# Kernel tuning notes

Measured on AMD Instinct MI355X. Metric: run time of the kernel, lower is better.

Reference implementation:

```python
import jax, jax.numpy as jnp
import numpy as np

N, D1, D2, BW, B = 8, 1024, 1024, 3, 1024
D = D1 * D2
RES_DENOS = [3.0, 5.0, 17.0, 257.0, 65537.0]  # [2^2-1, 2^2+1, 2^4+1, 2^8+1, 2^16+1]
SPLIT_TEMP = 0.01


def ste_floor(x):
    # forward: floor, backward: identity (matches custom round autograd.Function)
    return x + jax.lax.stop_gradient(jnp.floor(x) - x)


def quantize_weights(U, thres_mean):
    beta, alpha = jnp.max(U), jnp.min(U)
    s = (beta - alpha) / RES_DENOS[0]
    vals_sum = s * ste_floor(U / s)  # level 0
    col = jnp.arange(D)[None, :]
    for idx in range(1, BW):
        s = s / RES_DENOS[idx]
        res_err = U - vals_sum                                   # [N, D]
        order = jnp.argsort(res_err, axis=0)                     # [N, D] int
        sorted_err = jnp.take_along_axis(res_err, order, axis=0) # [N, D]
        delta = sorted_err[1:] - sorted_err[:-1]                 # [N-1, D]
        delta = delta / jnp.max(delta)
        # differentiable split points, one per gap between sorted rows
        sp = jax.nn.sigmoid((jnp.mean(delta, axis=1) - jax.nn.sigmoid(thres_mean)[0]) / SPLIT_TEMP)  # [N-1]
        b = jnp.round(sp)                                        # hard 0/1 boundary (zero grad, like torch branch)
        gid = jnp.concatenate([jnp.zeros((1,), sp.dtype), jnp.cumsum(b)]).astype(jnp.int32)  # [N] group id per row
        counts = jax.ops.segment_sum(jnp.ones((N,), U.dtype), gid, num_segments=N)           # [N]
        sums = jax.ops.segment_sum(sorted_err, gid, num_segments=N)                          # [N, D]
        means = sums / jnp.maximum(counts, 1.0)[:, None]
        # grad_ factor: sp at boundary rows, (1-sp) at interior rows, 1 for the last row
        factors = jnp.where(b == 1.0, sp, 1.0 - sp)              # [N-1], in (0,1)
        logf = jnp.concatenate([jnp.log(factors), jnp.zeros((1,), sp.dtype)])  # [N]
        grad_g = jnp.exp(jax.ops.segment_sum(logf, gid, num_segments=N))       # [N] per-group product
        t = grad_g[gid][:, None] * means[gid]                    # [N, D] group value broadcast to member rows
        # scatter back through the sort permutation (== one-hot transfer matmul)
        grouped = jnp.zeros_like(U).at[order, col].set(t)
        vals_sum = vals_sum + s * ste_floor(grouped / s)
    return vals_sum


def setup_inputs() -> dict:
    key = jax.random.key(0)
    kx, ku = jax.random.split(key)
    x = jax.random.normal(kx, (B, N, D1), dtype=jnp.float32)
    # kaiming_normal_ on (N, D): std = sqrt(2 / fan_in) with fan_in = D
    U = jax.random.normal(ku, (N, D), dtype=jnp.float32) * np.sqrt(2.0 / D).astype(np.float32)
    thres_mean = jnp.array([-0.405], dtype=jnp.float32)
    return {"x": x, "U": U, "thres_mean": thres_mean}


def reference(x, U, thres_mean):
    w = quantize_weights(U, thres_mean).reshape(N, D1, D2)
    return jnp.einsum('bnd,ndl->bnl', x, w)
```

## Files before the change

### kernel.cpp

```cpp
#include <hip/hip_runtime.h>
#include <hip/hip_bf16.h>
#include <stdint.h>

#define DD (1 << 20)
#define NPART 4096

typedef float v4f __attribute__((ext_vector_type(4)));
typedef __bf16 bf16x8 __attribute__((ext_vector_type(8)));

struct Scalars {
  float s;
  int   uniform;
  float coef[8];
  float cnti[8];
  int   isend[8];
};

struct Partial {
  double g[7];
  double mx;
};

static __device__ __forceinline__ unsigned short f2bf(float v) {
  unsigned u = __float_as_uint(v);
  u += 0x7fffu + ((u >> 16) & 1u);
  return (unsigned short)(u >> 16);
}

__global__ void k_minmax_partial(const float4* __restrict__ U4, float2* __restrict__ part) {
  int tid = threadIdx.x, bid = blockIdx.x;
  float mn = 3.4e38f, mx = -3.4e38f;
#pragma unroll
  for (int j = 0; j < 8; ++j) {
    float4 v = U4[(size_t)(bid * 8 + j) * 256 + tid];
    mn = fminf(mn, fminf(fminf(v.x, v.y), fminf(v.z, v.w)));
    mx = fmaxf(mx, fmaxf(fmaxf(v.x, v.y), fmaxf(v.z, v.w)));
  }
#pragma unroll
  for (int off = 32; off; off >>= 1) {
    mn = fminf(mn, __shfl_down(mn, off, 64));
    mx = fmaxf(mx, __shfl_down(mx, off, 64));
  }
  __shared__ float2 w4[4];
  if ((tid & 63) == 0) w4[tid >> 6] = make_float2(mn, mx);
  __syncthreads();
  if (tid == 0) {
    for (int i = 1; i < 4; ++i) { mn = fminf(mn, w4[i].x); mx = fmaxf(mx, w4[i].y); }
    part[bid] = make_float2(mn, mx);
  }
}

__global__ void k_minmax_final(const float2* __restrict__ part, Scalars* sc) {
  int tid = threadIdx.x;
  float mn = 3.4e38f, mx = -3.4e38f;
#pragma unroll
  for (int j = 0; j < 4; ++j) {
    float2 p = part[j * 256 + tid];
    mn = fminf(mn, p.x); mx = fmaxf(mx, p.y);
  }
#pragma unroll
  for (int off = 32; off; off >>= 1) {
    mn = fminf(mn, __shfl_down(mn, off, 64));
    mx = fmaxf(mx, __shfl_down(mx, off, 64));
  }
  __shared__ float2 w4[4];
  if ((tid & 63) == 0) w4[tid >> 6] = make_float2(mn, mx);
  __syncthreads();
  if (tid == 0) {
    for (int i = 1; i < 4; ++i) { mn = fminf(mn, w4[i].x); mx = fmaxf(mx, w4[i].y); }
    sc->s = (mx - mn) / 3.0f;
  }
}

#define CE2(a, b)                                                        \
  { float ra = r[a], rb = r[b]; int oa = ord[a], ob = ord[b];            \
    bool sw = (ra > rb) || (ra == rb && oa > ob);                        \
    r[a] = sw ? rb : ra; r[b] = sw ? ra : rb;                            \
    ord[a] = sw ? ob : oa; ord[b] = sw ? oa : ob; }

#define SORTNET8                                                          \
  CE2(0,1) CE2(2,3) CE2(4,5) CE2(6,7)                                     \
  CE2(0,2) CE2(1,3) CE2(4,6) CE2(5,7)                                     \
  CE2(1,2) CE2(5,6)                                                       \
  CE2(0,4) CE2(1,5) CE2(2,6) CE2(3,7)                                     \
  CE2(2,4) CE2(3,5)                                                       \
  CE2(1,2) CE2(3,4) CE2(5,6)

#define CEV(a, b) { float ra = q[a], rb = q[b]; q[a] = fminf(ra, rb); q[b] = fmaxf(ra, rb); }
#define SORTNET8V                                                         \
  CEV(0,1) CEV(2,3) CEV(4,5) CEV(6,7)                                     \
  CEV(0,2) CEV(1,3) CEV(4,6) CEV(5,7)                                     \
  CEV(1,2) CEV(5,6)                                                       \
  CEV(0,4) CEV(1,5) CEV(2,6) CEV(3,7)                                     \
  CEV(2,4) CEV(3,5)                                                       \
  CEV(1,2) CEV(3,4) CEV(5,6)

static __device__ __forceinline__ void stats_block_reduce(float dl[7], float mx,
                                                          Partial* __restrict__ po) {
#pragma unroll
  for (int off = 32; off; off >>= 1) {
#pragma unroll
    for (int g = 0; g < 7; ++g) dl[g] += __shfl_down(dl[g], off, 64);
    mx = fmaxf(mx, __shfl_down(mx, off, 64));
  }
  __shared__ double wsum[4][7];
  __shared__ float wmax[4];
  int lane = threadIdx.x & 63, wv = threadIdx.x >> 6;
  if (lane == 0) {
#pragma unroll
    for (int g = 0; g < 7; ++g) wsum[wv][g] = (double)dl[g];
    wmax[wv] = mx;
  }
  __syncthreads();
  if (threadIdx.x == 0) {
#pragma unroll
    for (int g = 0; g < 7; ++g)
      po->g[g] = wsum[0][g] + wsum[1][g] + wsum[2][g] + wsum[3][g];
    po->mx = (double)fmaxf(fmaxf(wmax[0], wmax[1]), fmaxf(wmax[2], wmax[3]));
  }
}

__global__ void k_level0_stats(const float* __restrict__ U, float* __restrict__ vals,
                               Partial* __restrict__ part, const Scalars* __restrict__ sc) {
  int d = blockIdx.x * 256 + threadIdx.x;
  float s = sc->s;
  float q[8];
#pragma unroll
  for (int n = 0; n < 8; ++n) {
    size_t ix = ((size_t)n << 20) + d;
    float u = U[ix];
    float v = s * floorf(u / s);
    vals[ix] = v;
    q[n] = u - v;
  }
  SORTNET8V
  float dl[7]; float mx = 0.f;
#pragma unroll
  for (int g = 0; g < 7; ++g) { dl[g] = q[g + 1] - q[g]; mx = fmaxf(mx, dl[g]); }
  stats_block_reduce(dl, mx, &part[blockIdx.x]);
}

__global__ void k_scalars2(const Partial* __restrict__ part, Scalars* sc,
                           const float* __restrict__ thres, float deno) {
  int t = threadIdx.x;
  double g[7] = {0, 0, 0, 0, 0, 0, 0};
  double mx = 0.0;
#pragma unroll
  for (int j = 0; j < NPART / 256; ++j) {
    const Partial& p = part[j * 256 + t];
#pragma unroll
    for (int i = 0; i < 7; ++i) g[i] += p.g[i];
    mx = fmax(mx, p.mx);
  }
#pragma unroll
  for (int off = 32; off; off >>= 1) {
#pragma unroll
    for (int i = 0; i < 7; ++i) g[i] += __shfl_down(g[i], off, 64);
    mx = fmax(mx, __shfl_down(mx, off, 64));
  }
  __shared__ double sg[4][8];
  int lane = t & 63, wv = t >> 6;
  if (lane == 0) {
#pragma unroll
    for (int i = 0; i < 7; ++i) sg[wv][i] = g[i];
    sg[wv][7] = mx;
  }
  __syncthreads();
  if (t != 0) return;
#pragma unroll
  for (int i = 0; i < 7; ++i) g[i] = sg[0][i] + sg[1][i] + sg[2][i] + sg[3][i];
  mx = fmax(fmax(sg[0][7], sg[1][7]), fmax(sg[2][7], sg[3][7]));

  float s = sc->s / deno;
  sc->s = s;
  float md = (float)mx;
  float sigT = 1.f / (1.f + expf(-thres[0]));
  float sp[7], bb[7];
  for (int gg = 0; gg < 7; ++gg) {
    float mean = (float)(g[gg] / ((double)DD * (double)md));
    float z = (mean - sigT) / 0.01f;
    sp[gg] = 1.f / (1.f + expf(-z));
    bb[gg] = rintf(sp[gg]);
  }
  int gid[8]; gid[0] = 0;
  for (int i = 1; i < 8; ++i) gid[i] = gid[i - 1] + (int)bb[i - 1];
  float counts[8] = {0, 0, 0, 0, 0, 0, 0, 0};
  for (int i = 0; i < 8; ++i) counts[gid[i]] += 1.f;
  float lsum[8] = {0, 0, 0, 0, 0, 0, 0, 0};
  for (int i = 0; i < 7; ++i) {
    float f = (bb[i] == 1.f) ? sp[i] : (1.f - sp[i]);
    lsum[gid[i]] += logf(f);
  }
  float gradg[8];
  for (int gg = 0; gg < 8; ++gg) gradg[gg] = expf(lsum[gg]);
  for (int i = 0; i < 8; ++i) {
    sc->coef[i] = gradg[gid[i]];
    sc->cnti[i] = fmaxf(counts[gid[i]], 1.f);
    sc->isend[i] = (i == 7) || (gid[i + 1] != gid[i]);
  }
  sc->uniform = (gid[7] == 0) ? 1 : 0;
}

static __device__ __forceinline__ void update_core(const float u[8], const float vo[8],
                                                   const float coef[8], const float cnti[8],
                                                   const int isend[8], float s,
                                                   float vnew[8]) {
  float r[8]; int ord[8];
#pragma unroll
  for (int n = 0; n < 8; ++n) { r[n] = u[n] - vo[n]; ord[n] = n; }
  SORTNET8
  float endsum[8]; float a = 0.f;
#pragma unroll
  for (int i = 0; i < 8; ++i) { a += r[i]; endsum[i] = a; if (isend[i]) a = 0.f; }
  float t[8]; float gsv = 0.f;
#pragma unroll
  for (int i = 7; i >= 0; --i) {
    if (isend[i]) gsv = endsum[i];
    t[i] = coef[i] * (gsv / cnti[i]);
  }
#pragma unroll
  for (int n = 0; n < 8; ++n) {
    float tv = 0.f;
#pragma unroll
    for (int i = 0; i < 8; ++i) tv = (ord[i] == n) ? t[i] : tv;
    vnew[n] = vo[n] + s * floorf(tv / s);
  }
}

static __device__ __forceinline__ float uniform_delta(const float u[8], const float vo[8],
                                                      float coef0, float cnt0, float s) {
  float q[8];
#pragma unroll
  for (int n = 0; n < 8; ++n) q[n] = u[n] - vo[n];
  SORTNET8V
  float a = 0.f;
#pragma unroll
  for (int i = 0; i < 8; ++i) a += q[i];
  float t = coef0 * (a / cnt0);
  return s * floorf(t / s);
}

__global__ void k_update_stats(const float* __restrict__ U, float* __restrict__ vals,
                               Partial* __restrict__ part, const Scalars* __restrict__ sc) {
  int d = blockIdx.x * 256 + threadIdx.x;
  float s = sc->s;
  float u[8], vo[8], vnew[8];
#pragma unroll
  for (int n = 0; n < 8; ++n) {
    size_t ix = ((size_t)n << 20) + d;
    u[n] = U[ix];
    vo[n] = vals[ix];
  }
  if (sc->uniform) {
    float c = uniform_delta(u, vo, sc->coef[0], sc->cnti[0], s);
#pragma unroll
    for (int n = 0; n < 8; ++n) vnew[n] = vo[n] + c;
  } else {
    float coef[8], cnti[8]; int isend[8];
#pragma unroll
    for (int i = 0; i < 8; ++i) { coef[i] = sc->coef[i]; cnti[i] = sc->cnti[i]; isend[i] = sc->isend[i]; }
    update_core(u, vo, coef, cnti, isend, s, vnew);
  }
  float q[8];
#pragma unroll
  for (int n = 0; n < 8; ++n) {
    size_t ix = ((size_t)n << 20) + d;
    vals[ix] = vnew[n];
    q[n] = u[n] - vnew[n];
  }
  SORTNET8V
  float dl[7]; float mx = 0.f;
#pragma unroll
  for (int g = 0; g < 7; ++g) { dl[g] = q[g + 1] - q[g]; mx = fmaxf(mx, dl[g]); }
  stats_block_reduce(dl, mx, &part[blockIdx.x]);
}

__global__ void k_final_pack(const float* __restrict__ x, const float* __restrict__ U,
                             const float* __restrict__ vals, const Scalars* __restrict__ sc,
                             unsigned short* __restrict__ xT, unsigned short* __restrict__ wT) {
  __shared__ unsigned short stile[8][32][34];
  int t = threadIdx.x;
  if (blockIdx.x < 1024) {
    int k0 = (blockIdx.x >> 5) * 32;
    int l0 = (blockIdx.x & 31) * 32;
    float s = sc->s;
    int uni = sc->uniform;
    float coef0 = sc->coef[0], cnt0 = sc->cnti[0];
    int kk = t >> 3;
    int lq = t & 7;
    int d0 = (k0 + kk) * 1024 + l0 + lq * 4;
    float4 u4[8], vo4[8];
#pragma unroll
    for (int n = 0; n < 8; ++n) {
      u4[n]  = *(const float4*)(U    + ((size_t)n << 20) + d0);
      vo4[n] = *(const float4*)(vals + ((size_t)n << 20) + d0);
    }
    if (uni) {
#pragma unroll
      for (int j = 0; j < 4; ++j) {
        float u[8], vo[8];
#pragma unroll
        for (int n = 0; n < 8; ++n) { u[n] = ((const float*)&u4[n])[j]; vo[n] = ((const float*)&vo4[n])[j]; }
        float c = uniform_delta(u, vo, coef0, cnt0, s);
#pragma unroll
        for (int n = 0; n < 8; ++n) stile[n][kk][lq * 4 + j] = f2bf(vo[n] + c);
      }
    } else {
      float coef[8], cnti[8]; int isend[8];
#pragma unroll
      for (int i = 0; i < 8; ++i) { coef[i] = sc->coef[i]; cnti[i] = sc->cnti[i]; isend[i] = sc->isend[i]; }
#pragma unroll
      for (int j = 0; j < 4; ++j) {
        float u[8], vo[8], vnew[8];
#pragma unroll
        for (int n = 0; n < 8; ++n) { u[n] = ((const float*)&u4[n])[j]; vo[n] = ((const float*)&vo4[n])[j]; }
        update_core(u, vo, coef, cnti, isend, s, vnew);
#pragma unroll
        for (int n = 0; n < 8; ++n) stile[n][kk][lq * 4 + j] = f2bf(vnew[n]);
      }
    }
    __syncthreads();
    int ll = t >> 3, kq = t & 7;
#pragma unroll
    for (int n = 0; n < 8; ++n) {
      ushort4 o;
      o.x = stile[n][kq * 4 + 0][ll];
      o.y = stile[n][kq * 4 + 1][ll];
      o.z = stile[n][kq * 4 + 2][ll];
      o.w = stile[n][kq * 4 + 3][ll];
      *(ushort4*)(wT + ((size_t)n << 20) + (size_t)(l0 + ll) * 1024 + k0 + kq * 4) = o;
    }
  } else {
    int bid2 = blockIdx.x - 1024;
#pragma unroll
    for (int j = 0; j < 4; ++j) {
      int i = j * (2048 * 256) + bid2 * 256 + t;
      int kq = i & 255;
      int b  = (i >> 8) & 1023;
      int n  = i >> 18;
      float4 v = *(const float4*)(x + ((size_t)(b * 8 + n) << 10) + (kq << 2));
      ushort4 o = make_ushort4(f2bf(v.x), f2bf(v.y), f2bf(v.z), f2bf(v.w));
      *(ushort4*)(xT + (((size_t)(n << 10 | b)) << 10) + (kq << 2)) = o;
    }
  }
}

__global__ __launch_bounds__(256, 2)
void k_gemm(const unsigned short* __restrict__ xT, const unsigned short* __restrict__ wT,
            float* __restrict__ out) {
  __shared__ bf16x8 sA[1024];
  __shared__ bf16x8 sB[1024];
  const int n  = blockIdx.x;
  const int m0 = blockIdx.y * 128;
  const int l0 = blockIdx.z * 128;
  const int tid = threadIdx.x;
  const int lane = tid & 63;
  const int wv = tid >> 6;
  const int wm = (wv & 1) * 64;
  const int wl = (wv >> 1) * 64;
  const unsigned short* A  = xT + ((size_t)n << 20);
  const unsigned short* Bt = wT + ((size_t)n << 20);

  v4f acc[4][4] = {};
  const int quad = lane >> 4;
  const int r16 = lane & 15;

  for (int kt = 0; kt < 1024; kt += 64) {
#pragma unroll
    for (int rr = 0; rr < 4; ++rr) {
      int cb = rr * 4 + wv;
      int c = cb * 64 + lane;
      int row = c >> 3;
      int gc = (c & 7) ^ (row & 7);
      const unsigned short* ga = A  + (size_t)(m0 + row) * 1024 + kt + gc * 8;
      const unsigned short* gb = Bt + (size_t)(l0 + row) * 1024 + kt + gc * 8;
      __builtin_amdgcn_global_load_lds((const __attribute__((address_space(1))) void*)ga,
                                       (__attribute__((address_space(3))) void*)&sA[cb * 64],
                                       16, 0, 0);
      __builtin_amdgcn_global_load_lds((const __attribute__((address_space(1))) void*)gb,
                                       (__attribute__((address_space(3))) void*)&sB[cb * 64],
                                       16, 0, 0);
    }
    asm volatile("s_waitcnt vmcnt(0)" ::: "memory");
    __syncthreads();

#pragma unroll
    for (int ks = 0; ks < 2; ++ks) {
      bf16x8 af[4], bfr[4];
#pragma unroll
      for (int t = 0; t < 4; ++t) {
        int arow = wm + t * 16 + r16;
        af[t] = sA[arow * 8 + ((ks * 4 + quad) ^ (arow & 7))];
        int brow = wl + t * 16 + r16;
        bfr[t] = sB[brow * 8 + ((ks * 4 + quad) ^ (brow & 7))];
      }
#pragma unroll
      for (int tm = 0; tm < 4; ++tm)
#pragma unroll
        for (int tn = 0; tn < 4; ++tn)
          acc[tm][tn] = __builtin_amdgcn_mfma_f32_16x16x32_bf16(af[tm], bfr[tn], acc[tm][tn], 0, 0, 0);
    }
    __syncthreads();
  }

#pragma unroll
  for (int tm = 0; tm < 4; ++tm)
#pragma unroll
    for (int tn = 0; tn < 4; ++tn)
#pragma unroll
      for (int rr = 0; rr < 4; ++rr) {
        int row = m0 + wm + tm * 16 + quad * 4 + rr;
        int col = l0 + wl + tn * 16 + r16;
        out[(size_t)(row * 8 + n) * 1024 + col] = acc[tm][tn][rr];
      }
}

extern "C" void kernel_launch(void* const* d_in, const int* in_sizes, int n_in,
                              void* d_out, int out_size, void* d_ws, size_t ws_size,
                              hipStream_t stream) {
  const float* x = (const float*)d_in[0];
  const float* U = (const float*)d_in[1];
  const float* thres = (const float*)d_in[2];
  float* out = (float*)d_out;

  char* w = (char*)d_ws;
  Scalars* sc = (Scalars*)w;
  float2* mmpart = (float2*)(w + 512);
  unsigned short* xT = (unsigned short*)(w + 16384);
  unsigned short* wT = xT + ((size_t)8 << 20);
  Partial* part = (Partial*)(w + 16384 + ((size_t)32 << 20));
  float* vals = out;

  k_minmax_partial<<<1024, 256, 0, stream>>>((const float4*)U, mmpart);
  k_minmax_final<<<1, 256, 0, stream>>>(mmpart, sc);
  k_level0_stats<<<NPART, 256, 0, stream>>>(U, vals, part, sc);
  k_scalars2<<<1, 256, 0, stream>>>(part, sc, thres, 5.0f);
  k_update_stats<<<NPART, 256, 0, stream>>>(U, vals, part, sc);
  k_scalars2<<<1, 256, 0, stream>>>(part, sc, thres, 17.0f);
  k_final_pack<<<3072, 256, 0, stream>>>(x, U, vals, sc, xT, wT);
  k_gemm<<<dim3(8, 8, 8), 256, 0, stream>>>(xT, wT, out);
}
```

Measured before the change: 201.6 us.

## Recompute quantization levels from U instead of storing intermediate vals buffer

Removes the intermediate vals array. Each pass now recomputes levels 0 and 1 from U using per-level scalar structs, instead of reading and writing 32 MB of fp32 state between kernels. The x-to-bf16 transpose moves from the final pack kernel into the first stats kernel, so it overlaps with level-0 statistics. In exchange, the final pack kernel does extra sort-network arithmetic to cut global memory traffic.

```diff
diff --git a/kernel.cpp b/kernel.cpp
--- a/kernel.cpp
+++ b/kernel.cpp
@@ -50,7 +50,7 @@
   }
 }
 
-__global__ void k_minmax_final(const float2* __restrict__ part, Scalars* sc) {
+__global__ void k_minmax_final(const float2* __restrict__ part, Scalars* sc0) {
   int tid = threadIdx.x;
   float mn = 3.4e38f, mx = -3.4e38f;
 #pragma unroll
@@ -68,7 +68,7 @@
   __syncthreads();
   if (tid == 0) {
     for (int i = 1; i < 4; ++i) { mn = fminf(mn, w4[i].x); mx = fmaxf(mx, w4[i].y); }
-    sc->s = (mx - mn) / 3.0f;
+    sc0->s = (mx - mn) / 3.0f;
   }
 }
 
@@ -120,91 +120,13 @@
   }
 }
 
-__global__ void k_level0_stats(const float* __restrict__ U, float* __restrict__ vals,
-                               Partial* __restrict__ part, const Scalars* __restrict__ sc) {
-  int d = blockIdx.x * 256 + threadIdx.x;
+static __device__ __forceinline__ void update_core(const float u[8], const float vo[8],
+                                                   const Scalars* __restrict__ sc,
+                                                   float vnew[8]) {
   float s = sc->s;
-  float q[8];
-#pragma unroll
-  for (int n = 0; n < 8; ++n) {
-    size_t ix = ((size_t)n << 20) + d;
-    float u = U[ix];
-    float v = s * floorf(u / s);
-    vals[ix] = v;
-    q[n] = u - v;
-  }
-  SORTNET8V
-  float dl[7]; float mx = 0.f;
-#pragma unroll
-  for (int g = 0; g < 7; ++g) { dl[g] = q[g + 1] - q[g]; mx = fmaxf(mx, dl[g]); }
-  stats_block_reduce(dl, mx, &part[blockIdx.x]);
-}
-
-__global__ void k_scalars2(const Partial* __restrict__ part, Scalars* sc,
-                           const float* __restrict__ thres, float deno) {
-  int t = threadIdx.x;
-  double g[7] = {0, 0, 0, 0, 0, 0, 0};
-  double mx = 0.0;
-#pragma unroll
-  for (int j = 0; j < NPART / 256; ++j) {
-    const Partial& p = part[j * 256 + t];
-#pragma unroll
-    for (int i = 0; i < 7; ++i) g[i] += p.g[i];
-    mx = fmax(mx, p.mx);
-  }
-#pragma unroll
-  for (int off = 32; off; off >>= 1) {
-#pragma unroll
-    for (int i = 0; i < 7; ++i) g[i] += __shfl_down(g[i], off, 64);
-    mx = fmax(mx, __shfl_down(mx, off, 64));
-  }
-  __shared__ double sg[4][8];
-  int lane = t & 63, wv = t >> 6;
-  if (lane == 0) {
-#pragma unroll
-    for (int i = 0; i < 7; ++i) sg[wv][i] = g[i];
-    sg[wv][7] = mx;
-  }
-  __syncthreads();
-  if (t != 0) return;
-#pragma unroll
-  for (int i = 0; i < 7; ++i) g[i] = sg[0][i] + sg[1][i] + sg[2][i] + sg[3][i];
-  mx = fmax(fmax(sg[0][7], sg[1][7]), fmax(sg[2][7], sg[3][7]));
-
-  float s = sc->s / deno;
-  sc->s = s;
-  float md = (float)mx;
-  float sigT = 1.f / (1.f + expf(-thres[0]));
-  float sp[7], bb[7];
-  for (int gg = 0; gg < 7; ++gg) {
-    float mean = (float)(g[gg] / ((double)DD * (double)md));
-    float z = (mean - sigT) / 0.01f;
-    sp[gg] = 1.f / (1.f + expf(-z));
-    bb[gg] = rintf(sp[gg]);
-  }
-  int gid[8]; gid[0] = 0;
-  for (int i = 1; i < 8; ++i) gid[i] = gid[i - 1] + (int)bb[i - 1];
-  float counts[8] = {0, 0, 0, 0, 0, 0, 0, 0};
-  for (int i = 0; i < 8; ++i) counts[gid[i]] += 1.f;
-  float lsum[8] = {0, 0, 0, 0, 0, 0, 0, 0};
-  for (int i = 0; i < 7; ++i) {
-    float f = (bb[i] == 1.f) ? sp[i] : (1.f - sp[i]);
-    lsum[gid[i]] += logf(f);
-  }
-  float gradg[8];
-  for (int gg = 0; gg < 8; ++gg) gradg[gg] = expf(lsum[gg]);
-  for (int i = 0; i < 8; ++i) {
-    sc->coef[i] = gradg[gid[i]];
-    sc->cnti[i] = fmaxf(counts[gid[i]], 1.f);
-    sc->isend[i] = (i == 7) || (gid[i + 1] != gid[i]);
-  }
-  sc->uniform = (gid[7] == 0) ? 1 : 0;
-}
-
-static __device__ __forceinline__ void update_core(const float u[8], const float vo[8],
-                                                   const float coef[8], const float cnti[8],
-                                                   const int isend[8], float s,
-                                                   float vnew[8]) {
+  float coef[8], cnti[8]; int isend[8];
+#pragma unroll
+  for (int i = 0; i < 8; ++i) { coef[i] = sc->coef[i]; cnti[i] = sc->cnti[i]; isend[i] = sc->isend[i]; }
   float r[8]; int ord[8];
 #pragma unroll
   for (int n = 0; n < 8; ++n) { r[n] = u[n] - vo[n]; ord[n] = n; }
@@ -240,98 +162,38 @@
   return s * floorf(t / s);
 }
 
-__global__ void k_update_stats(const float* __restrict__ U, float* __restrict__ vals,
-                               Partial* __restrict__ part, const Scalars* __restrict__ sc) {
-  int d = blockIdx.x * 256 + threadIdx.x;
-  float s = sc->s;
-  float u[8], vo[8], vnew[8];
-#pragma unroll
-  for (int n = 0; n < 8; ++n) {
-    size_t ix = ((size_t)n << 20) + d;
-    u[n] = U[ix];
-    vo[n] = vals[ix];
-  }
+static __device__ __forceinline__ void apply_update(const float u[8], const float vo[8],
+                                                    const Scalars* __restrict__ sc,
+                                                    float vnew[8]) {
   if (sc->uniform) {
-    float c = uniform_delta(u, vo, sc->coef[0], sc->cnti[0], s);
+    float c = uniform_delta(u, vo, sc->coef[0], sc->cnti[0], sc->s);
 #pragma unroll
     for (int n = 0; n < 8; ++n) vnew[n] = vo[n] + c;
   } else {
-    float coef[8], cnti[8]; int isend[8];
-#pragma unroll
-    for (int i = 0; i < 8; ++i) { coef[i] = sc->coef[i]; cnti[i] = sc->cnti[i]; isend[i] = sc->isend[i]; }
-    update_core(u, vo, coef, cnti, isend, s, vnew);
-  }
-  float q[8];
-#pragma unroll
-  for (int n = 0; n < 8; ++n) {
-    size_t ix = ((size_t)n << 20) + d;
-    vals[ix] = vnew[n];
-    q[n] = u[n] - vnew[n];
-  }
-  SORTNET8V
-  float dl[7]; float mx = 0.f;
-#pragma unroll
-  for (int g = 0; g < 7; ++g) { dl[g] = q[g + 1] - q[g]; mx = fmaxf(mx, dl[g]); }
-  stats_block_reduce(dl, mx, &part[blockIdx.x]);
-}
-
-__global__ void k_final_pack(const float* __restrict__ x, const float* __restrict__ U,
-                             const float* __restrict__ vals, const Scalars* __restrict__ sc,
-                             unsigned short* __restrict__ xT, unsigned short* __restrict__ wT) {
-  __shared__ unsigned short stile[8][32][34];
+    update_core(u, vo, sc, vnew);
+  }
+}
+
+__global__ void k_stats0(const float* __restrict__ U, Partial* __restrict__ part,
+                         const Scalars* __restrict__ sc0,
+                         const float* __restrict__ x, unsigned short* __restrict__ xT) {
   int t = threadIdx.x;
-  if (blockIdx.x < 1024) {
-    int k0 = (blockIdx.x >> 5) * 32;
-    int l0 = (blockIdx.x & 31) * 32;
-    float s = sc->s;
-    int uni = sc->uniform;
-    float coef0 = sc->coef[0], cnt0 = sc->cnti[0];
-    int kk = t >> 3;
-    int lq = t & 7;
-    int d0 = (k0 + kk) * 1024 + l0 + lq * 4;
-    float4 u4[8], vo4[8];
+  if (blockIdx.x < NPART) {
+    int d = blockIdx.x * 256 + t;
+    float s = sc0->s;
+    float q[8];
 #pragma unroll
     for (int n = 0; n < 8; ++n) {
-      u4[n]  = *(const float4*)(U    + ((size_t)n << 20) + d0);
-      vo4[n] = *(const float4*)(vals + ((size_t)n << 20) + d0);
+      float u = U[((size_t)n << 20) + d];
+      q[n] = u - s * floorf(u / s);
     }
-    if (uni) {
-#pragma unroll
-      for (int j = 0; j < 4; ++j) {
-        float u[8], vo[8];
-#pragma unroll
-        for (int n = 0; n < 8; ++n) { u[n] = ((const float*)&u4[n])[j]; vo[n] = ((const float*)&vo4[n])[j]; }
-        float c = uniform_delta(u, vo, coef0, cnt0, s);
-#pragma unroll
-        for (int n = 0; n < 8; ++n) stile[n][kk][lq * 4 + j] = f2bf(vo[n] + c);
-      }
-    } else {
-      float coef[8], cnti[8]; int isend[8];
-#pragma unroll
-      for (int i = 0; i < 8; ++i) { coef[i] = sc->coef[i]; cnti[i] = sc->cnti[i]; isend[i] = sc->isend[i]; }
-#pragma unroll
-      for (int j = 0; j < 4; ++j) {
-        float u[8], vo[8], vnew[8];
-#pragma unroll
-        for (int n = 0; n < 8; ++n) { u[n] = ((const float*)&u4[n])[j]; vo[n] = ((const float*)&vo4[n])[j]; }
-        update_core(u, vo, coef, cnti, isend, s, vnew);
-#pragma unroll
-        for (int n = 0; n < 8; ++n) stile[n][kk][lq * 4 + j] = f2bf(vnew[n]);
-      }
-    }
-    __syncthreads();
-    int ll = t >> 3, kq = t & 7;
-#pragma unroll
-    for (int n = 0; n < 8; ++n) {
-      ushort4 o;
-      o.x = stile[n][kq * 4 + 0][ll];
-      o.y = stile[n][kq * 4 + 1][ll];
-      o.z = stile[n][kq * 4 + 2][ll];
-      o.w = stile[n][kq * 4 + 3][ll];
-      *(ushort4*)(wT + ((size_t)n << 20) + (size_t)(l0 + ll) * 1024 + k0 + kq * 4) = o;
-    }
+    SORTNET8V
+    float dl[7]; float mx = 0.f;
+#pragma unroll
+    for (int g = 0; g < 7; ++g) { dl[g] = q[g + 1] - q[g]; mx = fmaxf(mx, dl[g]); }
+    stats_block_reduce(dl, mx, &part[blockIdx.x]);
   } else {
-    int bid2 = blockIdx.x - 1024;
+    int bid2 = blockIdx.x - NPART;
 #pragma unroll
     for (int j = 0; j < 4; ++j) {
       int i = j * (2048 * 256) + bid2 * 256 + t;
@@ -342,6 +204,129 @@
       ushort4 o = make_ushort4(f2bf(v.x), f2bf(v.y), f2bf(v.z), f2bf(v.w));
       *(ushort4*)(xT + (((size_t)(n << 10 | b)) << 10) + (kq << 2)) = o;
     }
+  }
+}
+
+__global__ void k_scalars2(const Partial* __restrict__ part, const Scalars* __restrict__ scin,
+                           Scalars* __restrict__ scout, const float* __restrict__ thres,
+                           float deno) {
+  int t = threadIdx.x;
+  double g[7] = {0, 0, 0, 0, 0, 0, 0};
+  double mx = 0.0;
+#pragma unroll
+  for (int j = 0; j < NPART / 256; ++j) {
+    const Partial& p = part[j * 256 + t];
+#pragma unroll
+    for (int i = 0; i < 7; ++i) g[i] += p.g[i];
+    mx = fmax(mx, p.mx);
+  }
+#pragma unroll
+  for (int off = 32; off; off >>= 1) {
+#pragma unroll
+    for (int i = 0; i < 7; ++i) g[i] += __shfl_down(g[i], off, 64);
+    mx = fmax(mx, __shfl_down(mx, off, 64));
+  }
+  __shared__ double sg[4][8];
+  int lane = t & 63, wv = t >> 6;
+  if (lane == 0) {
+#pragma unroll
+    for (int i = 0; i < 7; ++i) sg[wv][i] = g[i];
+    sg[wv][7] = mx;
+  }
+  __syncthreads();
+  if (t != 0) return;
+#pragma unroll
+  for (int i = 0; i < 7; ++i) g[i] = sg[0][i] + sg[1][i] + sg[2][i] + sg[3][i];
+  mx = fmax(fmax(sg[0][7], sg[1][7]), fmax(sg[2][7], sg[3][7]));
+
+  float s = scin->s / deno;
+  scout->s = s;
+  float md = (float)mx;
+  float sigT = 1.f / (1.f + expf(-thres[0]));
+  float sp[7], bb[7];
+  for (int gg = 0; gg < 7; ++gg) {
+    float mean = (float)(g[gg] / ((double)DD * (double)md));
+    float z = (mean - sigT) / 0.01f;
+    sp[gg] = 1.f / (1.f + expf(-z));
+    bb[gg] = rintf(sp[gg]);
+  }
+  int gid[8]; gid[0] = 0;
+  for (int i = 1; i < 8; ++i) gid[i] = gid[i - 1] + (int)bb[i - 1];
+  float counts[8] = {0, 0, 0, 0, 0, 0, 0, 0};
+  for (int i = 0; i < 8; ++i) counts[gid[i]] += 1.f;
+  float lsum[8] = {0, 0, 0, 0, 0, 0, 0, 0};
+  for (int i = 0; i < 7; ++i) {
+    float f = (bb[i] == 1.f) ? sp[i] : (1.f - sp[i]);
+    lsum[gid[i]] += logf(f);
+  }
+  float gradg[8];
+  for (int gg = 0; gg < 8; ++gg) gradg[gg] = expf(lsum[gg]);
+  for (int i = 0; i < 8; ++i) {
+    scout->coef[i] = gradg[gid[i]];
+    scout->cnti[i] = fmaxf(counts[gid[i]], 1.f);
+    scout->isend[i] = (i == 7) || (gid[i + 1] != gid[i]);
+  }
+  scout->uniform = (gid[7] == 0) ? 1 : 0;
+}
+
+__global__ void k_stats1(const float* __restrict__ U, Partial* __restrict__ part,
+                         const Scalars* __restrict__ sc0, const Scalars* __restrict__ sc1) {
+  int d = blockIdx.x * 256 + threadIdx.x;
+  float s0 = sc0->s;
+  float u[8], v0[8], v1[8];
+#pragma unroll
+  for (int n = 0; n < 8; ++n) {
+    u[n] = U[((size_t)n << 20) + d];
+    v0[n] = s0 * floorf(u[n] / s0);
+  }
+  apply_update(u, v0, sc1, v1);
+  float q[8];
+#pragma unroll
+  for (int n = 0; n < 8; ++n) q[n] = u[n] - v1[n];
+  SORTNET8V
+  float dl[7]; float mx = 0.f;
+#pragma unroll
+  for (int g = 0; g < 7; ++g) { dl[g] = q[g + 1] - q[g]; mx = fmaxf(mx, dl[g]); }
+  stats_block_reduce(dl, mx, &part[blockIdx.x]);
+}
+
+__global__ void k_final_pack(const float* __restrict__ U,
+                             const Scalars* __restrict__ sc0, const Scalars* __restrict__ sc1,
+                             const Scalars* __restrict__ sc2, unsigned short* __restrict__ wT) {
+  __shared__ unsigned short stile[8][32][34];
+  int t = threadIdx.x;
+  int k0 = (blockIdx.x >> 5) * 32;
+  int l0 = (blockIdx.x & 31) * 32;
+  float s0 = sc0->s;
+  int kk = t >> 3;
+  int lq = t & 7;
+  int d0 = (k0 + kk) * 1024 + l0 + lq * 4;
+  float4 u4[8];
+#pragma unroll
+  for (int n = 0; n < 8; ++n) u4[n] = *(const float4*)(U + ((size_t)n << 20) + d0);
+#pragma unroll
+  for (int j = 0; j < 4; ++j) {
+    float u[8], v0[8], v1[8], v2[8];
+#pragma unroll
+    for (int n = 0; n < 8; ++n) {
+      u[n] = ((const float*)&u4[n])[j];
+      v0[n] = s0 * floorf(u[n] / s0);
+    }
+    apply_update(u, v0, sc1, v1);
+    apply_update(u, v1, sc2, v2);
+#pragma unroll
+    for (int n = 0; n < 8; ++n) stile[n][kk][lq * 4 + j] = f2bf(v2[n]);
+  }
+  __syncthreads();
+  int ll = t >> 3, kq = t & 7;
+#pragma unroll
+  for (int n = 0; n < 8; ++n) {
+    ushort4 o;
+    o.x = stile[n][kq * 4 + 0][ll];
+    o.y = stile[n][kq * 4 + 1][ll];
+    o.z = stile[n][kq * 4 + 2][ll];
+    o.w = stile[n][kq * 4 + 3][ll];
+    *(ushort4*)(wT + ((size_t)n << 20) + (size_t)(l0 + ll) * 1024 + k0 + kq * 4) = o;
   }
 }
 
@@ -425,18 +410,17 @@
 
   char* w = (char*)d_ws;
   Scalars* sc = (Scalars*)w;
-  float2* mmpart = (float2*)(w + 512);
+  float2* mmpart = (float2*)(w + 4096);
   unsigned short* xT = (unsigned short*)(w + 16384);
   unsigned short* wT = xT + ((size_t)8 << 20);
   Partial* part = (Partial*)(w + 16384 + ((size_t)32 << 20));
-  float* vals = out;
 
   k_minmax_partial<<<1024, 256, 0, stream>>>((const float4*)U, mmpart);
-  k_minmax_final<<<1, 256, 0, stream>>>(mmpart, sc);
-  k_level0_stats<<<NPART, 256, 0, stream>>>(U, vals, part, sc);
-  k_scalars2<<<1, 256, 0, stream>>>(part, sc, thres, 5.0f);
-  k_update_stats<<<NPART, 256, 0, stream>>>(U, vals, part, sc);
-  k_scalars2<<<1, 256, 0, stream>>>(part, sc, thres, 17.0f);
-  k_final_pack<<<3072, 256, 0, stream>>>(x, U, vals, sc, xT, wT);
+  k_minmax_final<<<1, 256, 0, stream>>>(mmpart, &sc[0]);
+  k_stats0<<<NPART + 2048, 256, 0, stream>>>(U, part, &sc[0], x, xT);
+  k_scalars2<<<1, 256, 0, stream>>>(part, &sc[0], &sc[1], thres, 5.0f);
+  k_stats1<<<NPART, 256, 0, stream>>>(U, part, &sc[0], &sc[1]);
+  k_scalars2<<<1, 256, 0, stream>>>(part, &sc[1], &sc[2], thres, 17.0f);
+  k_final_pack<<<1024, 256, 0, stream>>>(U, &sc[0], &sc[1], &sc[2], wT);
   k_gemm<<<dim3(8, 8, 8), 256, 0, stream>>>(xT, wT, out);
 }
```

New measurement: 188.1 us. 6.7% less time.
